# Optimization experiments

Measured on AMD Instinct MI355X. Metric: run time of the kernel, lower is better.

Reference implementation:

```python
import jax
import jax.numpy as jnp
import numpy as np

TIME_DIVISION = 2
FILL_DIST = 50000.0  # sentinel initial distance, as in the torch module


def setup_inputs() -> dict:
    key = jax.random.key(0)
    k1, k2 = jax.random.split(key)
    B, T, H, W, C = 4, 16, 28, 28, 35
    TT = T // TIME_DIVISION
    x = jax.random.normal(k1, (B, T, H, W, C), dtype=jnp.float32)
    init_ = jax.random.randint(k2, (B * TIME_DIVISION,), 0, TT * H * W, dtype=jnp.int64)
    return {"x": x, "init_": init_, "k": 256}


def _pairwise_dist(xf):
    # xf: (Bt, N, C) -> (Bt, N, N) euclidean distances (torch.cdist p=2)
    sq = jnp.sum(xf * xf, axis=-1)                      # (Bt, N)
    gram = jnp.einsum('bnc,bmc->bnm', xf, xf)           # (Bt, N, N)
    d2 = jnp.maximum(sq[:, :, None] + sq[:, None, :] - 2.0 * gram, 0.0)
    return jnp.sqrt(d2)


def reference(x, init_, k):
    B, T, H, W, C = x.shape
    TT = T // TIME_DIVISION
    N = TT * H * W                 # points per time segment
    Bt = B * TIME_DIVISION
    k_ = k // TIME_DIVISION

    xf = x.reshape(Bt, N, C)
    cdist = _pairwise_dist(xf)
    # set diagonal to -1 (self-distance excluded from argmax)
    diag = jnp.arange(N)
    cdist = cdist.at[:, diag, diag].set(-1.0)

    b_idx = jnp.arange(Bt)
    farthest0 = jnp.remainder(init_, N)
    distance0 = jnp.full((Bt, N), FILL_DIST, dtype=x.dtype)

    def step(carry, _):
        distance, farthest = carry
        dist = cdist[b_idx, farthest]                   # (Bt, N) gather rows
        distance = jnp.minimum(dist, distance)
        farthest = jnp.argmax(distance, axis=-1)
        return (distance, farthest), farthest

    _, rest = jax.lax.scan(step, (distance0, farthest0), None, length=k_ - 1)
    sampling_index = jnp.concatenate([farthest0[None], rest], axis=0).T  # (Bt, k_)

    # add per-time-segment index offsets, flatten to (B, td*k_)
    offsets = (jnp.arange(TIME_DIVISION) * (TT * H * W))[None, :, None]
    sampling_index = sampling_index.reshape(B, TIME_DIVISION, k_) + offsets
    sampling_index = sampling_index.reshape(B, TIME_DIVISION * k_)

    # gather feature channels (first C-3; last 3 are positional encodings)
    xflat = x.reshape(B, T * H * W, C)
    patches = xflat[jnp.arange(B)[:, None], sampling_index][:, :, : C - 3]
    return patches, sampling_index
```

## Files before the change

kernel.cpp:

```cpp
#include <hip/hip_runtime.h>


#define NPTS 6272
#define CDIM 35
#define BT   8
#define KSEL 128
#define THW  12544
#define BPS  16
#define PPB  392
#define BLK  256
#define NB   (BT * BPS)
#define TAILN (PPB - BLK)

__device__ __forceinline__ unsigned long long key_of(float v, int j) {
  unsigned int u = __float_as_uint(v);
  u = (u & 0x80000000u) ? ~u : (u | 0x80000000u);
  return ((unsigned long long)u << 32) | (unsigned int)(NPTS - j);
}
__device__ __forceinline__ unsigned long long kmax(unsigned long long a,
                                                   unsigned long long b) {
  return a > b ? a : b;
}

template <int CTRL, int RMASK, bool BC>
__device__ __forceinline__ unsigned long long dpp_kmax(unsigned long long k) {
  unsigned int lo = (unsigned int)k, hi = (unsigned int)(k >> 32);
  unsigned int tlo = (unsigned int)__builtin_amdgcn_update_dpp(0, (int)lo, CTRL, RMASK, 0xF, BC);
  unsigned int thi = (unsigned int)__builtin_amdgcn_update_dpp(0, (int)hi, CTRL, RMASK, 0xF, BC);
  unsigned long long t = ((unsigned long long)thi << 32) | tlo;
  return kmax(k, t);
}
__device__ __forceinline__ unsigned long long wave_kmax64(unsigned long long k) {
  k = dpp_kmax<0x111, 0xF, true >(k);
  k = dpp_kmax<0x112, 0xF, true >(k);
  k = dpp_kmax<0x114, 0xF, true >(k);
  k = dpp_kmax<0x118, 0xF, true >(k);
  k = dpp_kmax<0x142, 0xA, false>(k);
  k = dpp_kmax<0x143, 0xC, false>(k);
  unsigned int rlo = (unsigned int)__builtin_amdgcn_readlane((int)(unsigned int)k, 63);
  unsigned int rhi = (unsigned int)__builtin_amdgcn_readlane((int)(k >> 32), 63);
  return ((unsigned long long)rhi << 32) | rlo;
}
__device__ __forceinline__ unsigned long long row16_kmax(unsigned long long k) {
  k = dpp_kmax<0x111, 0xF, true>(k);
  k = dpp_kmax<0x112, 0xF, true>(k);
  k = dpp_kmax<0x114, 0xF, true>(k);
  k = dpp_kmax<0x118, 0xF, true>(k);
  unsigned int rlo = (unsigned int)__builtin_amdgcn_readlane((int)(unsigned int)k, 15);
  unsigned int rhi = (unsigned int)__builtin_amdgcn_readlane((int)(k >> 32), 15);
  return ((unsigned long long)rhi << 32) | rlo;
}

__device__ __forceinline__ unsigned long long poll_slot(const unsigned long long* p) {
  unsigned int klo = 0u, khi = 0u;
  unsigned int a0, b0, a1, b1, a2, b2, t;
  asm volatile(
      "global_load_dword %[a0], %[ad], off sc0 sc1\n\t"
      "global_load_dword %[b0], %[ad], off offset:4 sc0 sc1\n\t"
      "global_load_dword %[a1], %[ad], off sc0 sc1\n\t"
      "global_load_dword %[b1], %[ad], off offset:4 sc0 sc1\n\t"
      "global_load_dword %[a2], %[ad], off sc0 sc1\n\t"
      "global_load_dword %[b2], %[ad], off offset:4 sc0 sc1\n\t"
      "1:\n\t"
      "s_waitcnt vmcnt(4)\n\t"
      "v_max_u32 %[klo], %[klo], %[a0]\n\t"
      "v_max_u32 %[khi], %[khi], %[b0]\n\t"
      "global_load_dword %[a0], %[ad], off sc0 sc1\n\t"
      "global_load_dword %[b0], %[ad], off offset:4 sc0 sc1\n\t"
      "v_min_u32 %[t], %[klo], %[khi]\n\t"
      "v_cmp_eq_u32 vcc, 0, %[t]\n\t"
      "s_cbranch_vccz 9f\n\t"
      "s_waitcnt vmcnt(4)\n\t"
      "v_max_u32 %[klo], %[klo], %[a1]\n\t"
      "v_max_u32 %[khi], %[khi], %[b1]\n\t"
      "global_load_dword %[a1], %[ad], off sc0 sc1\n\t"
      "global_load_dword %[b1], %[ad], off offset:4 sc0 sc1\n\t"
      "v_min_u32 %[t], %[klo], %[khi]\n\t"
      "v_cmp_eq_u32 vcc, 0, %[t]\n\t"
      "s_cbranch_vccz 9f\n\t"
      "s_waitcnt vmcnt(4)\n\t"
      "v_max_u32 %[klo], %[klo], %[a2]\n\t"
      "v_max_u32 %[khi], %[khi], %[b2]\n\t"
      "global_load_dword %[a2], %[ad], off sc0 sc1\n\t"
      "global_load_dword %[b2], %[ad], off offset:4 sc0 sc1\n\t"
      "v_min_u32 %[t], %[klo], %[khi]\n\t"
      "v_cmp_eq_u32 vcc, 0, %[t]\n\t"
      "s_cbranch_vccnz 1b\n\t"
      "9:\n\t"
      "s_waitcnt vmcnt(0)"
      : [klo] "+v"(klo), [khi] "+v"(khi),
        [a0] "=&v"(a0), [b0] "=&v"(b0), [a1] "=&v"(a1), [b1] "=&v"(b1),
        [a2] "=&v"(a2), [b2] "=&v"(b2), [t] "=&v"(t)
      : [ad] "v"(p)
      : "vcc", "memory");
  return ((unsigned long long)khi << 32) | klo;
}

__global__ __attribute__((amdgpu_waves_per_eu(1, 1))) __launch_bounds__(BLK)
void fps_kernel(const float* __restrict__ x,
                const int* __restrict__ init_,
                float* __restrict__ patches,
                float* __restrict__ sidx,
                unsigned long long* __restrict__ slots) {
  __shared__ unsigned long long wk[4];
  __shared__ int far_s;

  const int bid  = (int)blockIdx.x;
  const int b    = bid & 7;
  const int sub  = bid >> 3;
  const int tid  = (int)threadIdx.x;
  const int lane = tid & 63;
  const int wid  = tid >> 6;
  const int j0   = sub * PPB;
  const int td   = b & 1;
  const float* xg = x + (size_t)b * NPTS * CDIM;
  unsigned long long* seg = slots + (size_t)b * KSEL * BPS;

  float xr0[CDIM], xr1[CDIM];
  float sqr0, sqr1, df0, df1;
  {
    const float* src0 = xg + (size_t)(j0 + tid) * CDIM;
    float acc = 0.0f;
    {
#pragma clang fp contract(off)
#pragma unroll
      for (int c = 0; c < CDIM; ++c) { float v = src0[c]; xr0[c] = v; acc = acc + v * v; }
    }
    sqr0 = acc; df0 = 50000.0f;
    sqr1 = 0.0f; df1 = 50000.0f;
#pragma unroll
    for (int c = 0; c < CDIM; ++c) xr1[c] = 0.0f;
    if (tid < TAILN) {
      const float* src1 = xg + (size_t)(j0 + BLK + tid) * CDIM;
      float acc1 = 0.0f;
      {
#pragma clang fp contract(off)
#pragma unroll
        for (int c = 0; c < CDIM; ++c) { float v = src1[c]; xr1[c] = v; acc1 = acc1 + v * v; }
      }
      sqr1 = acc1;
    }
#pragma unroll
    for (int c = 0; c < CDIM; ++c) {
      asm volatile("" : "+v"(xr0[c]));
      asm volatile("" : "+v"(xr1[c]));
    }
    asm volatile("" : "+v"(sqr0));
    asm volatile("" : "+v"(sqr1));
  }

  int far;
  { int f = init_[b] % NPTS; if (f < 0) f += NPTS; far = f; }
  if (sub == 0 && wid == 1) {
    if (lane == 0) sidx[b * KSEL] = (float)(far + td * NPTS);
    if (lane < 32) patches[(size_t)(b * KSEL) * 32 + lane] = xg[(size_t)far * CDIM + lane];
  }

  for (int step = 1; step < KSEL; ++step) {
    const int fu = __builtin_amdgcn_readfirstlane(far);
    const float* fx = xg + (size_t)fu * CDIM;
    float xf[CDIM];
#pragma unroll
    for (int c = 0; c < CDIM; ++c) xf[c] = fx[c];

    float sqf;
    {
#pragma clang fp contract(off)
      float a = 0.0f;
#pragma unroll
      for (int c = 0; c < CDIM; ++c) { float t = xf[c]; a = a + t * t; }
      sqf = a;
    }

    unsigned long long bk;
    {
      float dot = 0.0f;
#pragma unroll
      for (int c = 0; c < CDIM; ++c)
        dot = __builtin_fmaf(xf[c], xr0[c], dot);
      float d2;
      {
#pragma clang fp contract(off)
        d2 = (sqf + sqr0) - 2.0f * dot;
      }
      d2 = fmaxf(d2, 0.0f);
      float d = __fsqrt_rn(d2);
      const int j = j0 + tid;
      d = (j == far) ? -1.0f : d;
      float nd = fminf(d, df0);
      df0 = nd;
      bk = key_of(nd, j);
    }
    if (tid < TAILN) {
      float dot = 0.0f;
#pragma unroll
      for (int c = 0; c < CDIM; ++c)
        dot = __builtin_fmaf(xf[c], xr1[c], dot);
      float d2;
      {
#pragma clang fp contract(off)
        d2 = (sqf + sqr1) - 2.0f * dot;
      }
      d2 = fmaxf(d2, 0.0f);
      float d = __fsqrt_rn(d2);
      const int j = j0 + BLK + tid;
      d = (j == far) ? -1.0f : d;
      float nd = fminf(d, df1);
      df1 = nd;
      bk = kmax(bk, key_of(nd, j));
    }

    bk = wave_kmax64(bk);
    if (lane == 0) wk[wid] = bk;
    __syncthreads();

    if (tid < BPS) {
      if (tid == 0) {
        unsigned long long m = kmax(kmax(wk[0], wk[1]), kmax(wk[2], wk[3]));
        __hip_atomic_store(&seg[step * BPS + sub], m,
                           __ATOMIC_RELAXED, __HIP_MEMORY_SCOPE_AGENT);
      }
      asm volatile("" ::: "memory");
      unsigned long long k = poll_slot(&seg[step * BPS + tid]);
      k = row16_kmax(k);
      if (tid == 0)
        far_s = NPTS - (int)(unsigned int)(k & 0xFFFFFFFFull);
    }
    __syncthreads();
    far = far_s;

    if (sub == 0 && wid == 1) {
      if (lane == 0) sidx[b * KSEL + step] = (float)(far + td * NPTS);
      if (lane < 32) patches[(size_t)(b * KSEL + step) * 32 + lane] =
                         xg[(size_t)far * CDIM + lane];
    }
  }
}

extern "C" void kernel_launch(void* const* d_in, const int* in_sizes, int n_in,
                              void* d_out, int out_size, void* d_ws, size_t ws_size,
                              hipStream_t stream) {
  const float* x    = (const float*)d_in[0];
  const int*   init = (const int*)d_in[1];
  (void)in_sizes; (void)n_in; (void)out_size; (void)ws_size;

  unsigned long long* slots = (unsigned long long*)d_ws;
  const size_t slots_bytes = (size_t)BT * KSEL * BPS * sizeof(unsigned long long);

  float* patches = (float*)d_out;
  float* sidx    = patches + (size_t)4 * 256 * 32;

  hipMemsetAsync(d_ws, 0, slots_bytes, stream);

  void* kargs[] = { (void*)&x, (void*)&init, (void*)&patches, (void*)&sidx,
                    (void*)&slots };
  hipLaunchCooperativeKernel((const void*)fps_kernel, dim3(NB), dim3(BLK),
                             kargs, 0, stream);
}
```

Baseline: 220.2 us.

## Speculate two FPS steps per exchange using top-2 candidate reduction

Each grid-wide exchange now reduces the top two keys per block along with a max key, so the runner-up can be guessed as the next farthest point. Each block computes distances for both the known new point and the speculative candidate, then checks whether the speculated max matches. On a hit, two selection steps finish with one cross-block exchange, roughly halving the global synchronisations. A miss falls back to an extra exchange, and every step now does more arithmetic and heavier reductions.

```diff
diff --git a/kernel.cpp b/kernel.cpp
--- a/kernel.cpp
+++ b/kernel.cpp
@@ -11,6 +11,7 @@
 #define BLK  256
 #define NB   (BT * BPS)
 #define TAILN (PPB - BLK)
+#define ROWS 128
 
 __device__ __forceinline__ unsigned long long key_of(float v, int j) {
   unsigned int u = __float_as_uint(v);
@@ -21,14 +22,36 @@
                                                    unsigned long long b) {
   return a > b ? a : b;
 }
+__device__ __forceinline__ unsigned long long kmin(unsigned long long a,
+                                                   unsigned long long b) {
+  return a < b ? a : b;
+}
+
+struct KPair { unsigned long long b, s; };
+__device__ __forceinline__ KPair pmerge(KPair x, KPair y) {
+  KPair r;
+  r.b = kmax(x.b, y.b);
+  r.s = kmax(kmin(x.b, y.b), kmax(x.s, y.s));
+  return r;
+}
 
 template <int CTRL, int RMASK, bool BC>
-__device__ __forceinline__ unsigned long long dpp_kmax(unsigned long long k) {
+__device__ __forceinline__ unsigned long long dpp_mov64(unsigned long long k) {
   unsigned int lo = (unsigned int)k, hi = (unsigned int)(k >> 32);
   unsigned int tlo = (unsigned int)__builtin_amdgcn_update_dpp(0, (int)lo, CTRL, RMASK, 0xF, BC);
   unsigned int thi = (unsigned int)__builtin_amdgcn_update_dpp(0, (int)hi, CTRL, RMASK, 0xF, BC);
-  unsigned long long t = ((unsigned long long)thi << 32) | tlo;
-  return kmax(k, t);
+  return ((unsigned long long)thi << 32) | tlo;
+}
+template <int CTRL, int RMASK, bool BC>
+__device__ __forceinline__ unsigned long long dpp_kmax(unsigned long long k) {
+  return kmax(k, dpp_mov64<CTRL, RMASK, BC>(k));
+}
+template <int CTRL, int RMASK, bool BC>
+__device__ __forceinline__ KPair dpp_pmerge(KPair p) {
+  KPair t;
+  t.b = dpp_mov64<CTRL, RMASK, BC>(p.b);
+  t.s = dpp_mov64<CTRL, RMASK, BC>(p.s);
+  return pmerge(p, t);
 }
 __device__ __forceinline__ unsigned long long wave_kmax64(unsigned long long k) {
   k = dpp_kmax<0x111, 0xF, true >(k);
@@ -41,14 +64,21 @@
   unsigned int rhi = (unsigned int)__builtin_amdgcn_readlane((int)(k >> 32), 63);
   return ((unsigned long long)rhi << 32) | rlo;
 }
-__device__ __forceinline__ unsigned long long row16_kmax(unsigned long long k) {
-  k = dpp_kmax<0x111, 0xF, true>(k);
-  k = dpp_kmax<0x112, 0xF, true>(k);
-  k = dpp_kmax<0x114, 0xF, true>(k);
-  k = dpp_kmax<0x118, 0xF, true>(k);
-  unsigned int rlo = (unsigned int)__builtin_amdgcn_readlane((int)(unsigned int)k, 15);
-  unsigned int rhi = (unsigned int)__builtin_amdgcn_readlane((int)(k >> 32), 15);
-  return ((unsigned long long)rhi << 32) | rlo;
+__device__ __forceinline__ KPair wave_preduce(KPair p) {
+  p = dpp_pmerge<0x111, 0xF, true >(p);
+  p = dpp_pmerge<0x112, 0xF, true >(p);
+  p = dpp_pmerge<0x114, 0xF, true >(p);
+  p = dpp_pmerge<0x118, 0xF, true >(p);
+  p = dpp_pmerge<0x142, 0xA, false>(p);
+  p = dpp_pmerge<0x143, 0xC, false>(p);
+  unsigned int blo = (unsigned int)__builtin_amdgcn_readlane((int)(unsigned int)p.b, 63);
+  unsigned int bhi = (unsigned int)__builtin_amdgcn_readlane((int)(p.b >> 32), 63);
+  unsigned int slo = (unsigned int)__builtin_amdgcn_readlane((int)(unsigned int)p.s, 63);
+  unsigned int shi = (unsigned int)__builtin_amdgcn_readlane((int)(p.s >> 32), 63);
+  KPair r;
+  r.b = ((unsigned long long)bhi << 32) | blo;
+  r.s = ((unsigned long long)shi << 32) | slo;
+  return r;
 }
 
 __device__ __forceinline__ unsigned long long poll_slot(const unsigned long long* p) {
@@ -96,14 +126,54 @@
   return ((unsigned long long)khi << 32) | klo;
 }
 
+struct ExRes { unsigned long long maxkc, g1, g2; };
+
+__device__ __forceinline__ ExRes do_exchange(
+    unsigned long long* seg, int row, KPair pp, unsigned long long kk,
+    int sub, int tid, int lane, int wid,
+    unsigned long long* wk, unsigned long long* wb, unsigned long long* wsec,
+    unsigned long long* res) {
+  unsigned long long kcw = wave_kmax64(kk);
+  KPair pw = wave_preduce(pp);
+  if (lane == 0) { wk[wid] = kcw; wb[wid] = pw.b; wsec[wid] = pw.s; }
+  __syncthreads();
+  if (tid == 0) {
+    unsigned long long KC = kmax(kmax(wk[0], wk[1]), kmax(wk[2], wk[3]));
+    KPair P0{wb[0], wsec[0]}, P1{wb[1], wsec[1]}, P2{wb[2], wsec[2]}, P3{wb[3], wsec[3]};
+    KPair P = pmerge(pmerge(P0, P1), pmerge(P2, P3));
+    unsigned long long* slot = seg + (size_t)row * 64 + sub * 4;
+    __hip_atomic_store(slot + 0, P.b, __ATOMIC_RELAXED, __HIP_MEMORY_SCOPE_AGENT);
+    __hip_atomic_store(slot + 1, P.s, __ATOMIC_RELAXED, __HIP_MEMORY_SCOPE_AGENT);
+    __hip_atomic_store(slot + 2, KC,  __ATOMIC_RELAXED, __HIP_MEMORY_SCOPE_AGENT);
+  }
+  asm volatile("" ::: "memory");
+  if (wid == 0) {
+    unsigned long long kv = 0ull;
+    if (lane < 48)
+      kv = poll_slot(seg + (size_t)row * 64 + (lane & 15) * 4 + (lane >> 4));
+    unsigned long long kcv = (lane >= 32) ? kv : 0ull;
+    kcv = wave_kmax64(kcv);
+    KPair q{(lane < 32) ? kv : 0ull, 0ull};
+    q = wave_preduce(q);
+    if (lane == 0) { res[0] = kcv; res[1] = q.b; res[2] = q.s; }
+  }
+  __syncthreads();
+  ExRes r;
+  r.maxkc = res[0]; r.g1 = res[1]; r.g2 = res[2];
+  return r;
+}
+
+__device__ __forceinline__ int key_idx(unsigned long long k) {
+  return NPTS - (int)(unsigned int)(k & 0xFFFFFFFFull);
+}
+
 __global__ __attribute__((amdgpu_waves_per_eu(1, 1))) __launch_bounds__(BLK)
 void fps_kernel(const float* __restrict__ x,
                 const int* __restrict__ init_,
                 float* __restrict__ patches,
                 float* __restrict__ sidx,
                 unsigned long long* __restrict__ slots) {
-  __shared__ unsigned long long wk[4];
-  __shared__ int far_s;
+  __shared__ unsigned long long wk[4], wb[4], wsec[4], res[3];
 
   const int bid  = (int)blockIdx.x;
   const int b    = bid & 7;
@@ -111,15 +181,16 @@
   const int tid  = (int)threadIdx.x;
   const int lane = tid & 63;
   const int wid  = tid >> 6;
-  const int j0   = sub * PPB;
+  const int j0t  = sub * PPB + tid;
+  const int j1t  = sub * PPB + BLK + tid;
   const int td   = b & 1;
   const float* xg = x + (size_t)b * NPTS * CDIM;
-  unsigned long long* seg = slots + (size_t)b * KSEL * BPS;
+  unsigned long long* seg = slots + (size_t)b * ROWS * 64;
 
   float xr0[CDIM], xr1[CDIM];
   float sqr0, sqr1, df0, df1;
   {
-    const float* src0 = xg + (size_t)(j0 + tid) * CDIM;
+    const float* src0 = xg + (size_t)j0t * CDIM;
     float acc = 0.0f;
     {
 #pragma clang fp contract(off)
@@ -131,7 +202,7 @@
 #pragma unroll
     for (int c = 0; c < CDIM; ++c) xr1[c] = 0.0f;
     if (tid < TAILN) {
-      const float* src1 = xg + (size_t)(j0 + BLK + tid) * CDIM;
+      const float* src1 = xg + (size_t)j1t * CDIM;
       float acc1 = 0.0f;
       {
 #pragma clang fp contract(off)
@@ -149,92 +220,176 @@
     asm volatile("" : "+v"(sqr1));
   }
 
-  int far;
-  { int f = init_[b] % NPTS; if (f < 0) f += NPTS; far = f; }
+  int w;
+  { int f = init_[b] % NPTS; if (f < 0) f += NPTS; w = f; }
   if (sub == 0 && wid == 1) {
-    if (lane == 0) sidx[b * KSEL] = (float)(far + td * NPTS);
-    if (lane < 32) patches[(size_t)(b * KSEL) * 32 + lane] = xg[(size_t)far * CDIM + lane];
-  }
-
-  for (int step = 1; step < KSEL; ++step) {
-    const int fu = __builtin_amdgcn_readfirstlane(far);
-    const float* fx = xg + (size_t)fu * CDIM;
-    float xf[CDIM];
-#pragma unroll
-    for (int c = 0; c < CDIM; ++c) xf[c] = fx[c];
-
-    float sqf;
+    if (lane == 0) sidx[b * KSEL] = (float)(w + td * NPTS);
+    if (lane < 32) patches[(size_t)(b * KSEL) * 32 + lane] = xg[(size_t)w * CDIM + lane];
+  }
+
+  unsigned long long cK = 0;
+  int cidx = 0;
+  int row = 0;
+
+#define CERTAIN_TAIL(SQF, DW0, DW1, CEN)                                   \
+  {                                                                        \
+    float d2a;                                                             \
+    { _Pragma("clang fp contract(off)") d2a = (SQF + sqr0) - 2.0f * DW0; } \
+    d2a = fmaxf(d2a, 0.0f);                                                \
+    float da = __fsqrt_rn(d2a);                                            \
+    da = (j0t == (CEN)) ? -1.0f : da;                                      \
+    df0 = fminf(da, df0);                                                  \
+    if (tid < TAILN) {                                                     \
+      float d2b;                                                           \
+      { _Pragma("clang fp contract(off)") d2b = (SQF + sqr1) - 2.0f * DW1; } \
+      d2b = fmaxf(d2b, 0.0f);                                              \
+      float db = __fsqrt_rn(d2b);                                          \
+      db = (j1t == (CEN)) ? -1.0f : db;                                    \
+      df1 = fminf(db, df1);                                                \
+    }                                                                      \
+  }
+
+  {
+    const int wu = __builtin_amdgcn_readfirstlane(w);
+    const float* fx = xg + (size_t)wu * CDIM;
+    float xfw[CDIM];
+#pragma unroll
+    for (int c = 0; c < CDIM; ++c) xfw[c] = fx[c];
+    float sqfw;
     {
 #pragma clang fp contract(off)
       float a = 0.0f;
 #pragma unroll
-      for (int c = 0; c < CDIM; ++c) { float t = xf[c]; a = a + t * t; }
-      sqf = a;
-    }
-
-    unsigned long long bk;
+      for (int c = 0; c < CDIM; ++c) { float t = xfw[c]; a = a + t * t; }
+      sqfw = a;
+    }
+    float dw0 = 0.0f, dw1 = 0.0f;
+#pragma unroll
+    for (int c = 0; c < CDIM; ++c) {
+      dw0 = __builtin_fmaf(xfw[c], xr0[c], dw0);
+      dw1 = __builtin_fmaf(xfw[c], xr1[c], dw1);
+    }
+    CERTAIN_TAIL(sqfw, dw0, dw1, w)
+    unsigned long long kA = key_of(df0, j0t);
+    unsigned long long kB = (tid < TAILN) ? key_of(df1, j1t) : 0ull;
+    KPair pp{kmax(kA, kB), kmin(kA, kB)};
+    ExRes r = do_exchange(seg, row, pp, pp.b, sub, tid, lane, wid, wk, wb, wsec, res);
+    ++row;
+    int far1 = key_idx(r.g1);
+    if (sub == 0 && wid == 1) {
+      if (lane == 0) sidx[b * KSEL + 1] = (float)(far1 + td * NPTS);
+      if (lane < 32) patches[(size_t)(b * KSEL + 1) * 32 + lane] =
+                         xg[(size_t)far1 * CDIM + lane];
+    }
+    w = far1; cK = r.g2; cidx = key_idx(r.g2);
+  }
+
+  for (int s = 2; s <= 126; s += 2) {
+    const int wu = __builtin_amdgcn_readfirstlane(w);
+    const int cu = __builtin_amdgcn_readfirstlane(cidx);
+    const float* fw = xg + (size_t)wu * CDIM;
+    const float* fc = xg + (size_t)cu * CDIM;
+    float xfw[CDIM], xfc[CDIM];
+#pragma unroll
+    for (int c = 0; c < CDIM; ++c) { xfw[c] = fw[c]; xfc[c] = fc[c]; }
+    float sqfw, sqfc;
     {
-      float dot = 0.0f;
-#pragma unroll
-      for (int c = 0; c < CDIM; ++c)
-        dot = __builtin_fmaf(xf[c], xr0[c], dot);
-      float d2;
+#pragma clang fp contract(off)
+      float a = 0.0f;
+#pragma unroll
+      for (int c = 0; c < CDIM; ++c) { float t = xfw[c]; a = a + t * t; }
+      sqfw = a;
+      float e = 0.0f;
+#pragma unroll
+      for (int c = 0; c < CDIM; ++c) { float t = xfc[c]; e = e + t * t; }
+      sqfc = e;
+    }
+    float dw0 = 0.0f, dw1 = 0.0f, dc0 = 0.0f, dc1 = 0.0f;
+#pragma unroll
+    for (int c = 0; c < CDIM; ++c) {
+      dw0 = __builtin_fmaf(xfw[c], xr0[c], dw0);
+      dc0 = __builtin_fmaf(xfc[c], xr0[c], dc0);
+      dw1 = __builtin_fmaf(xfw[c], xr1[c], dw1);
+      dc1 = __builtin_fmaf(xfc[c], xr1[c], dc1);
+    }
+    CERTAIN_TAIL(sqfw, dw0, dw1, w)
+    unsigned long long kk = key_of(df0, j0t);
+    if (tid < TAILN) kk = kmax(kk, key_of(df1, j1t));
+    float dfs0 = df0, dfs1 = df1;
+    {
+      float d2a;
+      { _Pragma("clang fp contract(off)") d2a = (sqfc + sqr0) - 2.0f * dc0; }
+      d2a = fmaxf(d2a, 0.0f);
+      float da = __fsqrt_rn(d2a);
+      da = (j0t == cidx) ? -1.0f : da;
+      dfs0 = fminf(da, df0);
+      if (tid < TAILN) {
+        float d2b;
+        { _Pragma("clang fp contract(off)") d2b = (sqfc + sqr1) - 2.0f * dc1; }
+        d2b = fmaxf(d2b, 0.0f);
+        float db = __fsqrt_rn(d2b);
+        db = (j1t == cidx) ? -1.0f : db;
+        dfs1 = fminf(db, df1);
+      }
+    }
+    unsigned long long kA = key_of(dfs0, j0t);
+    unsigned long long kB = (tid < TAILN) ? key_of(dfs1, j1t) : 0ull;
+    KPair pp{kmax(kA, kB), kmin(kA, kB)};
+
+    ExRes r = do_exchange(seg, row, pp, kk, sub, tid, lane, wid, wk, wb, wsec, res);
+    ++row;
+    int farS = key_idx(r.maxkc);
+    if (sub == 0 && wid == 1) {
+      if (lane == 0) sidx[b * KSEL + s] = (float)(farS + td * NPTS);
+      if (lane < 32) patches[(size_t)(b * KSEL + s) * 32 + lane] =
+                         xg[(size_t)farS * CDIM + lane];
+    }
+
+    if (r.maxkc == cK) {
+      df0 = dfs0; df1 = dfs1;
+      int farS1 = key_idx(r.g1);
+      if (sub == 0 && wid == 1) {
+        if (lane == 0) sidx[b * KSEL + s + 1] = (float)(farS1 + td * NPTS);
+        if (lane < 32) patches[(size_t)(b * KSEL + s + 1) * 32 + lane] =
+                           xg[(size_t)farS1 * CDIM + lane];
+      }
+      w = farS1; cK = r.g2; cidx = key_idx(r.g2);
+    } else {
+      const int eu = __builtin_amdgcn_readfirstlane(farS);
+      const float* fe = xg + (size_t)eu * CDIM;
+      float xfe[CDIM];
+#pragma unroll
+      for (int c = 0; c < CDIM; ++c) xfe[c] = fe[c];
+      float sqfe;
       {
 #pragma clang fp contract(off)
-        d2 = (sqf + sqr0) - 2.0f * dot;
-      }
-      d2 = fmaxf(d2, 0.0f);
-      float d = __fsqrt_rn(d2);
-      const int j = j0 + tid;
-      d = (j == far) ? -1.0f : d;
-      float nd = fminf(d, df0);
-      df0 = nd;
-      bk = key_of(nd, j);
-    }
-    if (tid < TAILN) {
-      float dot = 0.0f;
-#pragma unroll
-      for (int c = 0; c < CDIM; ++c)
-        dot = __builtin_fmaf(xf[c], xr1[c], dot);
-      float d2;
-      {
-#pragma clang fp contract(off)
-        d2 = (sqf + sqr1) - 2.0f * dot;
-      }
-      d2 = fmaxf(d2, 0.0f);
-      float d = __fsqrt_rn(d2);
-      const int j = j0 + BLK + tid;
-      d = (j == far) ? -1.0f : d;
-      float nd = fminf(d, df1);
-      df1 = nd;
-      bk = kmax(bk, key_of(nd, j));
-    }
-
-    bk = wave_kmax64(bk);
-    if (lane == 0) wk[wid] = bk;
-    __syncthreads();
-
-    if (tid < BPS) {
-      if (tid == 0) {
-        unsigned long long m = kmax(kmax(wk[0], wk[1]), kmax(wk[2], wk[3]));
-        __hip_atomic_store(&seg[step * BPS + sub], m,
-                           __ATOMIC_RELAXED, __HIP_MEMORY_SCOPE_AGENT);
-      }
-      asm volatile("" ::: "memory");
-      unsigned long long k = poll_slot(&seg[step * BPS + tid]);
-      k = row16_kmax(k);
-      if (tid == 0)
-        far_s = NPTS - (int)(unsigned int)(k & 0xFFFFFFFFull);
-    }
-    __syncthreads();
-    far = far_s;
-
-    if (sub == 0 && wid == 1) {
-      if (lane == 0) sidx[b * KSEL + step] = (float)(far + td * NPTS);
-      if (lane < 32) patches[(size_t)(b * KSEL + step) * 32 + lane] =
-                         xg[(size_t)far * CDIM + lane];
-    }
-  }
+        float a = 0.0f;
+#pragma unroll
+        for (int c = 0; c < CDIM; ++c) { float t = xfe[c]; a = a + t * t; }
+        sqfe = a;
+      }
+      float de0 = 0.0f, de1 = 0.0f;
+#pragma unroll
+      for (int c = 0; c < CDIM; ++c) {
+        de0 = __builtin_fmaf(xfe[c], xr0[c], de0);
+        de1 = __builtin_fmaf(xfe[c], xr1[c], de1);
+      }
+      CERTAIN_TAIL(sqfe, de0, de1, farS)
+      unsigned long long kA2 = key_of(df0, j0t);
+      unsigned long long kB2 = (tid < TAILN) ? key_of(df1, j1t) : 0ull;
+      KPair pp2{kmax(kA2, kB2), kmin(kA2, kB2)};
+      ExRes r2 = do_exchange(seg, row, pp2, pp2.b, sub, tid, lane, wid, wk, wb, wsec, res);
+      ++row;
+      int farS1 = key_idx(r2.g1);
+      if (sub == 0 && wid == 1) {
+        if (lane == 0) sidx[b * KSEL + s + 1] = (float)(farS1 + td * NPTS);
+        if (lane < 32) patches[(size_t)(b * KSEL + s + 1) * 32 + lane] =
+                           xg[(size_t)farS1 * CDIM + lane];
+      }
+      w = farS1; cK = r2.g2; cidx = key_idx(r2.g2);
+    }
+  }
+#undef CERTAIN_TAIL
 }
 
 extern "C" void kernel_launch(void* const* d_in, const int* in_sizes, int n_in,
@@ -245,7 +400,7 @@
   (void)in_sizes; (void)n_in; (void)out_size; (void)ws_size;
 
   unsigned long long* slots = (unsigned long long*)d_ws;
-  const size_t slots_bytes = (size_t)BT * KSEL * BPS * sizeof(unsigned long long);
+  const size_t slots_bytes = (size_t)BT * ROWS * 64 * sizeof(unsigned long long);
 
   float* patches = (float*)d_out;
   float* sidx    = patches + (size_t)4 * 256 * 32;
```

Measured after the change: 247.9 us. 12.5% more time.
